# Kernel optimization log

Measured on AMD Instinct MI355X. Metric: run time of the kernel, lower is better.

## Reference

```python
import jax, jax.numpy as jnp
import numpy as np

B, D, K, M1, M2 = 256, 128, 32, 64, 32   # batch, n_nodes, K copies, dims[1], dims[2]
H1, H2, L = 128, 64, 32                   # pivae_dims


def setup_inputs() -> dict:
    key = jax.random.key(0)
    ks = iter(jax.random.split(key, 32))

    def rn(shape, scale):
        return jax.random.normal(next(ks), shape, dtype=jnp.float32) * scale

    x = jax.random.normal(next(ks), (B, D), dtype=jnp.float32)

    # per-node fc1 weights: [D, M1, D]; bounds force nonneg with zero diag column
    W1_pos = jnp.abs(rn((D, M1, D), 1.0 / np.sqrt(D)))
    W1_neg = jnp.abs(rn((D, M1, D), 1.0 / np.sqrt(D)))
    eye = jnp.eye(D, dtype=jnp.float32)[:, None, :]   # zero out W[j,:,j]
    W1_pos = W1_pos * (1.0 - eye)
    W1_neg = W1_neg * (1.0 - eye)
    b1_pos = rn((D, M1), 0.02)
    b1_neg = rn((D, M1), 0.02)

    # LocallyConnected stacks: weight [K, m_in, m_out]
    lc1_w = rn((K, M1, M2), 1.0 / np.sqrt(M1)); lc1_b = rn((K, M2), 0.02)
    lc2_w = rn((K, M2, 1), 1.0 / np.sqrt(M2));  lc2_b = rn((K, 1), 0.02)

    # per-sample beta Linear(k,1): weights [B, K], bias [B]
    beta_w = rn((B, K), 1.0 / np.sqrt(K)); beta_b = rn((B,), 0.02)

    # VAE params (encoder -> mu/logvar -> decoder), stored as (in,out) matrices
    enc1_w = rn((K, H1), 1.0 / np.sqrt(K));  enc1_b = jnp.zeros((H1,), jnp.float32)
    enc2_w = rn((H1, H2), 1.0 / np.sqrt(H1)); enc2_b = jnp.zeros((H2,), jnp.float32)
    mu_w = rn((H2, L), 1.0 / np.sqrt(H2));    mu_b = jnp.zeros((L,), jnp.float32)
    lv_w = rn((H2, L), 1.0 / np.sqrt(H2));    lv_b = jnp.zeros((L,), jnp.float32)
    dec1_w = rn((L, H2), 1.0 / np.sqrt(L));   dec1_b = jnp.zeros((H2,), jnp.float32)
    dec2_w = rn((H2, H1), 1.0 / np.sqrt(H2)); dec2_b = jnp.zeros((H1,), jnp.float32)
    dec3_w = rn((H1, K), 1.0 / np.sqrt(H1));  dec3_b = jnp.zeros((K,), jnp.float32)

    eps = jax.random.normal(next(ks), (B, L), dtype=jnp.float32)  # reparam noise

    return dict(x=x, W1_pos=W1_pos, W1_neg=W1_neg, b1_pos=b1_pos, b1_neg=b1_neg,
                lc1_w=lc1_w, lc1_b=lc1_b, lc2_w=lc2_w, lc2_b=lc2_b,
                beta_w=beta_w, beta_b=beta_b,
                enc1_w=enc1_w, enc1_b=enc1_b, enc2_w=enc2_w, enc2_b=enc2_b,
                mu_w=mu_w, mu_b=mu_b, lv_w=lv_w, lv_b=lv_b,
                dec1_w=dec1_w, dec1_b=dec1_b, dec2_w=dec2_w, dec2_b=dec2_b,
                dec3_w=dec3_w, dec3_b=dec3_b, eps=eps)


def reference(x, W1_pos, W1_neg, b1_pos, b1_neg, lc1_w, lc1_b, lc2_w, lc2_b,
              beta_w, beta_b, enc1_w, enc1_b, enc2_w, enc2_b, mu_w, mu_b,
              lv_w, lv_b, dec1_w, dec1_b, dec2_w, dec2_b, dec3_w, dec3_b, eps):
    b, d = x.shape
    k = lc1_w.shape[0]

    # fused per-node fc1: (pos - neg) applied to x with column j zeroed, all j at once
    W1 = W1_pos - W1_neg                      # [D, M1, D]
    b1 = b1_pos - b1_neg                      # [D, M1]
    full = jnp.einsum('bi,jhi->bjh', x, W1)   # as if no column were zeroed
    diagW = jnp.einsum('jhj->jh', W1)         # [D, M1] column-j weight of node j
    phi = full - x[:, :, None] * diagW[None] + b1[None]   # [B, D, M1]

    # expand to K copies, run sigmoid + LocallyConnected stack
    h = jnp.broadcast_to(phi[:, :, None, :], (b, d, k, phi.shape[-1]))
    h = jnp.einsum('bdkm,kmn->bdkn', jax.nn.sigmoid(h), lc1_w) + lc1_b   # [B,D,K,M2]
    h = jnp.einsum('bdkm,kmn->bdkn', jax.nn.sigmoid(h), lc2_w) + lc2_b   # [B,D,K,1]
    last_phi_x = h[..., 0]                    # [B, D, K]

    # per-sample beta projection (batched over B)
    y1 = jnp.einsum('bdk,bk->bd', last_phi_x, beta_w) + beta_b[:, None]

    # VAE on the stacked beta weights [B, K]
    e = jax.nn.relu(beta_w @ enc1_w + enc1_b)
    e = jax.nn.relu(e @ enc2_w + enc2_b)
    mu = e @ mu_w + mu_b
    logvar = e @ lv_w + lv_b
    z = mu + eps * jnp.exp(0.5 * logvar)
    dh = jax.nn.relu(z @ dec1_w + dec1_b)
    dh = jax.nn.relu(dh @ dec2_w + dec2_b)
    recon = dh @ dec3_w + dec3_b              # [B, K]

    y2 = jnp.einsum('bdk,bk->bd', last_phi_x, recon) + beta_b[:, None]
    return (y1, y2, mu, logvar)
```

## Files before the change

kernel.cpp:

```cpp
#include <hip/hip_runtime.h>
#include <stdint.h>

#define BB 256
#define DD 128
#define KK 32
#define MM1 64
#define MM2 32

typedef __attribute__((ext_vector_type(8))) short bf16x8;
typedef __attribute__((ext_vector_type(4))) float f32x4;

__device__ __forceinline__ short f2b(float f) {
  uint32_t u = __builtin_bit_cast(uint32_t, f);
  u += 0x7FFFu + ((u >> 16) & 1u);
  return (short)(u >> 16);
}
__device__ __forceinline__ float sigmoidf_fast(float xv) {
  return __builtin_amdgcn_rcpf(1.0f + __expf(-xv));
}

__global__ __launch_bounds__(128) void vae_kernel(
    const float* __restrict__ betaw,
    const float* __restrict__ enc1w, const float* __restrict__ enc1b,
    const float* __restrict__ enc2w, const float* __restrict__ enc2b,
    const float* __restrict__ muw,  const float* __restrict__ mub,
    const float* __restrict__ lvw,  const float* __restrict__ lvb,
    const float* __restrict__ dec1w, const float* __restrict__ dec1b,
    const float* __restrict__ dec2w, const float* __restrict__ dec2b,
    const float* __restrict__ dec3w, const float* __restrict__ dec3b,
    const float* __restrict__ eps,
    float* __restrict__ mu_out, float* __restrict__ lv_out,
    float* __restrict__ recon_out)
{
  const int b = blockIdx.x, t = threadIdx.x;
  __shared__ float bw[KK], e1[128], e2[64], zz[32], d1s[64];
  if (t < KK) bw[t] = betaw[b * KK + t];
  __syncthreads();
  {
    float acc = enc1b[t];
    #pragma unroll
    for (int k = 0; k < KK; ++k) acc = fmaf(bw[k], enc1w[k * 128 + t], acc);
    e1[t] = fmaxf(acc, 0.f);
  }
  __syncthreads();
  if (t < 64) {
    float a2 = enc2b[t];
    #pragma unroll 8
    for (int h = 0; h < 128; ++h) a2 = fmaf(e1[h], enc2w[h * 64 + t], a2);
    e2[t] = fmaxf(a2, 0.f);
  }
  __syncthreads();
  if (t < 32) {
    float m = mub[t], l = lvb[t];
    #pragma unroll 8
    for (int h = 0; h < 64; ++h) {
      float e = e2[h];
      m = fmaf(e, muw[h * 32 + t], m);
      l = fmaf(e, lvw[h * 32 + t], l);
    }
    mu_out[b * 32 + t] = m;
    lv_out[b * 32 + t] = l;
    zz[t] = fmaf(eps[b * 32 + t], __expf(0.5f * l), m);
  }
  __syncthreads();
  if (t < 64) {
    float a3 = dec1b[t];
    #pragma unroll
    for (int l = 0; l < 32; ++l) a3 = fmaf(zz[l], dec1w[l * 64 + t], a3);
    d1s[t] = fmaxf(a3, 0.f);
  }
  __syncthreads();
  float d2v;
  {
    float a4 = dec2b[t];
    #pragma unroll 8
    for (int h = 0; h < 64; ++h) a4 = fmaf(d1s[h], dec2w[h * 128 + t], a4);
    d2v = fmaxf(a4, 0.f);
  }
  __syncthreads();
  __shared__ float d2s[128];
  d2s[t] = d2v;
  __syncthreads();
  if (t < 32) {
    float a5 = dec3b[t];
    #pragma unroll 8
    for (int h = 0; h < 128; ++h) a5 = fmaf(d2s[h], dec3w[h * 32 + t], a5);
    recon_out[b * 32 + t] = a5;
  }
}

__global__ __launch_bounds__(512) void main_kernel(
    const float* __restrict__ x,
    const float* __restrict__ W1p, const float* __restrict__ W1n,
    const float* __restrict__ b1p, const float* __restrict__ b1n,
    const float* __restrict__ lc1w, const float* __restrict__ lc1b,
    const float* __restrict__ lc2w, const float* __restrict__ lc2b,
    const float* __restrict__ betaw, const float* __restrict__ betab,
    const float* __restrict__ recon,
    float* __restrict__ out)
{
  const int bx = blockIdx.x;
  const int d = bx >> 1;
  const int b0 = (bx & 1) * 128;
  const int tid = threadIdx.x;
  const int wave = tid >> 6;
  const int lane = tid & 63;

  __shared__ __align__(16) short sS[128 * 64];
  __shared__ __align__(16) float betaS[128 * 32];
  __shared__ __align__(16) float reconS[128 * 32];
  __shared__ __align__(16) float lc2S[KK * MM2];
  __shared__ __align__(16) float lc1bS[KK * MM2];
  __shared__ float lc2bS[KK];
  __shared__ float b1S[MM1];
  __shared__ __align__(16) short uni[32768];

  {
    const float4* xsrc = (const float4*)(x + b0 * DD);
    for (int e = tid; e < 4096; e += 512) {
      float4 v = xsrc[e];
      int row = e >> 5;
      int i = (e & 31) * 4;
      int ib = i & ~7, il = i & 7;
      short4 o; o.x = f2b(v.x); o.y = f2b(v.y); o.z = f2b(v.z); o.w = f2b(v.w);
      *(short4*)&uni[row * 128 + (ib ^ ((row & 7) << 3)) + il] = o;
    }
    const float4* wp = (const float4*)(W1p + d * MM1 * DD);
    const float4* wn = (const float4*)(W1n + d * MM1 * DD);
    for (int e = tid; e < 2048; e += 512) {
      float4 p = wp[e], n = wn[e];
      int m = e >> 5;
      int i = (e & 31) * 4;
      int ib = i & ~7, il = i & 7;
      short4 o; o.x = f2b(p.x - n.x); o.y = f2b(p.y - n.y);
      o.z = f2b(p.z - n.z); o.w = f2b(p.w - n.w);
      *(short4*)&uni[16384 + m * 128 + (ib ^ ((m & 7) << 3)) + il] = o;
    }
    if (tid < MM1) b1S[tid] = b1p[d * MM1 + tid] - b1n[d * MM1 + tid];
    const float4* bws = (const float4*)(betaw + b0 * KK);
    const float4* rcs = (const float4*)(recon + b0 * KK);
    for (int e = tid; e < 1024; e += 512) {
      ((float4*)betaS)[e]  = bws[e];
      ((float4*)reconS)[e] = rcs[e];
    }
    if (tid < 256) {
      ((float4*)lc2S)[tid]  = ((const float4*)lc2w)[tid];
      ((float4*)lc1bS)[tid] = ((const float4*)lc1b)[tid];
    }
    if (tid < KK) lc2bS[tid] = lc2b[tid];
  }
  __syncthreads();

  {
    const int row = wave * 16 + (lane & 15);
    const int kof = (lane >> 4) * 8;
    const int rsw = (row & 7) << 3;
    bf16x8 a[4];
    #pragma unroll
    for (int ks = 0; ks < 4; ++ks)
      a[ks] = *(const bf16x8*)&uni[row * 128 + ((ks * 32 + kof) ^ rsw)];
    #pragma unroll
    for (int ct = 0; ct < 4; ++ct) {
      const int m = ct * 16 + (lane & 15);
      const int msw = (m & 7) << 3;
      f32x4 acc = {0.f, 0.f, 0.f, 0.f};
      #pragma unroll
      for (int ks = 0; ks < 4; ++ks) {
        bf16x8 bf = *(const bf16x8*)&uni[16384 + m * 128 + ((ks * 32 + kof) ^ msw)];
        acc = __builtin_amdgcn_mfma_f32_16x16x32_bf16(a[ks], bf, acc, 0, 0, 0);
      }
      const float bias = b1S[m];
      #pragma unroll
      for (int r = 0; r < 4; ++r) {
        int bb = wave * 16 + (lane >> 4) * 4 + r;
        float s = sigmoidf_fast(acc[r] + bias);
        int mhi = m & ~7, mlo = m & 7;
        sS[bb * 64 + (mhi ^ ((bb & 7) << 3)) + mlo] = f2b(s);
      }
    }
  }
  __syncthreads();

  float y1a[4] = {0, 0, 0, 0}, y2a[4] = {0, 0, 0, 0};
  bf16x8 sa[2];
  {
    const int row = wave * 16 + (lane & 15);
    const int kofl = (lane >> 4) * 8;
    const int rsw = (row & 7) << 3;
    sa[0] = *(const bf16x8*)&sS[row * 64 + ((0 + kofl) ^ rsw)];
    sa[1] = *(const bf16x8*)&sS[row * 64 + ((32 + kofl) ^ rsw)];
  }
  const int n0 = lane & 15;
  const int kof = (lane >> 4) * 8;
  #pragma unroll 1
  for (int kh = 0; kh < 2; ++kh) {
    __syncthreads();
    {
      const float* src = lc1w + kh * 32768;
      for (int e = tid; e < 32768; e += 512) {
        int kq = e >> 11;
        int m = (e >> 5) & 63;
        int n = e & 31;
        int cp = kq * 32 + n;
        uni[cp * 64 + ((m & ~7) ^ ((cp & 7) << 3)) + (m & 7)] = f2b(src[e]);
      }
    }
    __syncthreads();
    for (int kk = 0; kk < 16; ++kk) {
      const int k = kh * 16 + kk;
      const int c0 = kk * 32 + n0, c1 = c0 + 16;
      const float bi0 = lc1bS[k * 32 + n0], bi1 = lc1bS[k * 32 + n0 + 16];
      f32x4 acc0 = {bi0, bi0, bi0, bi0}, acc1 = {bi1, bi1, bi1, bi1};
      #pragma unroll
      for (int mh = 0; mh < 2; ++mh) {
        int mb = mh * 32 + kof;
        bf16x8 bf0 = *(const bf16x8*)&uni[c0 * 64 + (mb ^ ((c0 & 7) << 3))];
        bf16x8 bf1 = *(const bf16x8*)&uni[c1 * 64 + (mb ^ ((c1 & 7) << 3))];
        acc0 = __builtin_amdgcn_mfma_f32_16x16x32_bf16(sa[mh], bf0, acc0, 0, 0, 0);
        acc1 = __builtin_amdgcn_mfma_f32_16x16x32_bf16(sa[mh], bf1, acc1, 0, 0, 0);
      }
      const float w0 = lc2S[k * 32 + n0], w1 = lc2S[k * 32 + n0 + 16];
      float v[4];
      #pragma unroll
      for (int r = 0; r < 4; ++r)
        v[r] = fmaf(sigmoidf_fast(acc0[r]), w0, sigmoidf_fast(acc1[r]) * w1);
      #pragma unroll
      for (int msk = 1; msk <= 8; msk <<= 1) {
        #pragma unroll
        for (int r = 0; r < 4; ++r) v[r] += __shfl_xor(v[r], msk, 64);
      }
      const float l2b = lc2bS[k];
      #pragma unroll
      for (int r = 0; r < 4; ++r) {
        int bb = wave * 16 + (lane >> 4) * 4 + r;
        float h2 = v[r] + l2b;
        y1a[r] = fmaf(h2, betaS[bb * 32 + k], y1a[r]);
        y2a[r] = fmaf(h2, reconS[bb * 32 + k], y2a[r]);
      }
    }
  }

  if ((lane & 15) == 0) {
    #pragma unroll
    for (int r = 0; r < 4; ++r) {
      int row = b0 + wave * 16 + (lane >> 4) * 4 + r;
      float bconst = betab[row];
      out[row * DD + d] = y1a[r] + bconst;
      out[BB * DD + row * DD + d] = y2a[r] + bconst;
    }
  }
}

extern "C" void kernel_launch(void* const* d_in, const int* in_sizes, int n_in,
                              void* d_out, int out_size, void* d_ws, size_t ws_size,
                              hipStream_t stream) {
  const float* x     = (const float*)d_in[0];
  const float* W1p   = (const float*)d_in[1];
  const float* W1n   = (const float*)d_in[2];
  const float* b1p   = (const float*)d_in[3];
  const float* b1n   = (const float*)d_in[4];
  const float* lc1w  = (const float*)d_in[5];
  const float* lc1b  = (const float*)d_in[6];
  const float* lc2w  = (const float*)d_in[7];
  const float* lc2b  = (const float*)d_in[8];
  const float* betaw = (const float*)d_in[9];
  const float* betab = (const float*)d_in[10];
  const float* enc1w = (const float*)d_in[11];
  const float* enc1b = (const float*)d_in[12];
  const float* enc2w = (const float*)d_in[13];
  const float* enc2b = (const float*)d_in[14];
  const float* muw   = (const float*)d_in[15];
  const float* mub   = (const float*)d_in[16];
  const float* lvw   = (const float*)d_in[17];
  const float* lvb   = (const float*)d_in[18];
  const float* dec1w = (const float*)d_in[19];
  const float* dec1b = (const float*)d_in[20];
  const float* dec2w = (const float*)d_in[21];
  const float* dec2b = (const float*)d_in[22];
  const float* dec3w = (const float*)d_in[23];
  const float* dec3b = (const float*)d_in[24];
  const float* eps   = (const float*)d_in[25];

  float* out   = (float*)d_out;
  float* recon = (float*)d_ws;

  float* mu_out = out + BB * DD * 2;
  float* lv_out = mu_out + BB * 32;

  vae_kernel<<<dim3(BB), dim3(128), 0, stream>>>(
      betaw, enc1w, enc1b, enc2w, enc2b, muw, mub, lvw, lvb,
      dec1w, dec1b, dec2w, dec2b, dec3w, dec3b, eps,
      mu_out, lv_out, recon);

  main_kernel<<<dim3(256), dim3(512), 0, stream>>>(
      x, W1p, W1n, b1p, b1n, lc1w, lc1b, lc2w, lc2b,
      betaw, betab, recon, out);
}
```

Before: 166.4 us.

## Add prep kernel for bf16 conversions and restructure main kernel over finer grid

Adds a prep kernel that converts W1, x and lc1 weights to bf16 once, pre-transposes beta/recon, and folds biases into log2e-scaled constants so the sigmoid becomes a single exp2 plus rcp. The main kernel now runs 1024 blocks of 256 threads, each covering 32 batch rows per node. It splits the K dimension across waves, streams lc1 fragments straight from global memory with register double-buffering, and finishes with a cross-wave reduction in shared memory. This removes the redundant per-block conversion of lc1w and W1 into LDS. The costs are an extra launch, a workspace round trip, and more global/L2 traffic for the lc1 fragments.

```diff
diff --git a/kernel.cpp b/kernel.cpp
--- a/kernel.cpp
+++ b/kernel.cpp
@@ -10,13 +10,56 @@
 typedef __attribute__((ext_vector_type(8))) short bf16x8;
 typedef __attribute__((ext_vector_type(4))) float f32x4;
 
+#define LOG2E 1.44269504088896f
+
+
 __device__ __forceinline__ short f2b(float f) {
   uint32_t u = __builtin_bit_cast(uint32_t, f);
   u += 0x7FFFu + ((u >> 16) & 1u);
   return (short)(u >> 16);
 }
-__device__ __forceinline__ float sigmoidf_fast(float xv) {
-  return __builtin_amdgcn_rcpf(1.0f + __expf(-xv));
+__device__ __forceinline__ float sigm_pre(float acc, float cpre) {
+  return __builtin_amdgcn_rcpf(
+      1.0f + __builtin_amdgcn_exp2f(fmaf(acc, -LOG2E, cpre)));
+}
+
+__global__ __launch_bounds__(256) void prep_kernel(
+    const float* __restrict__ x, const float* __restrict__ W1p,
+    const float* __restrict__ W1n, const float* __restrict__ b1p,
+    const float* __restrict__ b1n, const float* __restrict__ lc1w,
+    const float* __restrict__ lc1b, const float* __restrict__ lc2b,
+    const float* __restrict__ betaw, char* __restrict__ ws)
+{
+  const int tid = blockIdx.x * 256 + threadIdx.x;
+
+  {
+    float4 a = ((const float4*)W1p)[tid];
+    float4 b = ((const float4*)W1n)[tid];
+    short4 s;
+    s.x = f2b(a.x - b.x); s.y = f2b(a.y - b.y);
+    s.z = f2b(a.z - b.z); s.w = f2b(a.w - b.w);
+    ((short4*)(ws + 303104))[tid] = s;
+  }
+  if (tid < 8192) {
+    float4 v = ((const float4*)x)[tid];
+    short4 s;
+    s.x = f2b(v.x); s.y = f2b(v.y); s.z = f2b(v.z); s.w = f2b(v.w);
+    ((short4*)(ws + 65536))[tid] = s;
+  }
+  if (tid < 65536) {
+    int k = tid >> 11, n = (tid >> 6) & 31, m = tid & 63;
+    ((short*)(ws + 131072))[tid] = f2b(lc1w[k * 2048 + m * 32 + n]);
+  }
+  if (tid < 8192) {
+    ((float*)(ws + 32768))[tid] = betaw[(tid & 255) * 32 + (tid >> 8)];
+  }
+  if (tid < 1024) {
+    ((float*)(ws + 262144))[tid] = -lc1b[tid] * LOG2E;
+  }
+  if (tid < 32) { ((float*)(ws + 266240))[tid] = 0.25f * lc2b[tid]; }
+  if (tid < 8192) {
+    ((float*)(ws + 270336))[tid] = -(b1p[tid] - b1n[tid]) * LOG2E;
+  }
 }
 
 __global__ __launch_bounds__(128) void vae_kernel(
@@ -30,224 +73,208 @@
     const float* __restrict__ dec3w, const float* __restrict__ dec3b,
     const float* __restrict__ eps,
     float* __restrict__ mu_out, float* __restrict__ lv_out,
-    float* __restrict__ recon_out)
+    float* __restrict__ reconT)
 {
   const int b = blockIdx.x, t = threadIdx.x;
-  __shared__ float bw[KK], e1[128], e2[64], zz[32], d1s[64];
+  __shared__ float bw[KK], e1[128], e2[64], zz[32], d1s[64], d2s[128];
   if (t < KK) bw[t] = betaw[b * KK + t];
   __syncthreads();
   {
-    float acc = enc1b[t];
+    float a0 = enc1b[t], a1 = 0.f;
     #pragma unroll
-    for (int k = 0; k < KK; ++k) acc = fmaf(bw[k], enc1w[k * 128 + t], acc);
-    e1[t] = fmaxf(acc, 0.f);
+    for (int k = 0; k < KK; k += 2) {
+      a0 = fmaf(bw[k], enc1w[k * 128 + t], a0);
+      a1 = fmaf(bw[k + 1], enc1w[(k + 1) * 128 + t], a1);
+    }
+    e1[t] = fmaxf(a0 + a1, 0.f);
   }
   __syncthreads();
   if (t < 64) {
-    float a2 = enc2b[t];
+    float a0 = enc2b[t], a1 = 0.f, a2 = 0.f, a3 = 0.f;
     #pragma unroll 8
-    for (int h = 0; h < 128; ++h) a2 = fmaf(e1[h], enc2w[h * 64 + t], a2);
-    e2[t] = fmaxf(a2, 0.f);
+    for (int h = 0; h < 128; h += 4) {
+      a0 = fmaf(e1[h], enc2w[h * 64 + t], a0);
+      a1 = fmaf(e1[h + 1], enc2w[(h + 1) * 64 + t], a1);
+      a2 = fmaf(e1[h + 2], enc2w[(h + 2) * 64 + t], a2);
+      a3 = fmaf(e1[h + 3], enc2w[(h + 3) * 64 + t], a3);
+    }
+    e2[t] = fmaxf((a0 + a1) + (a2 + a3), 0.f);
   }
   __syncthreads();
   if (t < 32) {
-    float m = mub[t], l = lvb[t];
+    float m0 = mub[t], m1 = 0.f, l0 = lvb[t], l1 = 0.f;
     #pragma unroll 8
-    for (int h = 0; h < 64; ++h) {
-      float e = e2[h];
-      m = fmaf(e, muw[h * 32 + t], m);
-      l = fmaf(e, lvw[h * 32 + t], l);
-    }
+    for (int h = 0; h < 64; h += 2) {
+      float ea = e2[h], eb = e2[h + 1];
+      m0 = fmaf(ea, muw[h * 32 + t], m0);
+      m1 = fmaf(eb, muw[(h + 1) * 32 + t], m1);
+      l0 = fmaf(ea, lvw[h * 32 + t], l0);
+      l1 = fmaf(eb, lvw[(h + 1) * 32 + t], l1);
+    }
+    float m = m0 + m1, l = l0 + l1;
     mu_out[b * 32 + t] = m;
     lv_out[b * 32 + t] = l;
     zz[t] = fmaf(eps[b * 32 + t], __expf(0.5f * l), m);
   }
   __syncthreads();
   if (t < 64) {
-    float a3 = dec1b[t];
+    float a0 = dec1b[t], a1 = 0.f;
     #pragma unroll
-    for (int l = 0; l < 32; ++l) a3 = fmaf(zz[l], dec1w[l * 64 + t], a3);
-    d1s[t] = fmaxf(a3, 0.f);
-  }
-  __syncthreads();
-  float d2v;
+    for (int l = 0; l < 32; l += 2) {
+      a0 = fmaf(zz[l], dec1w[l * 64 + t], a0);
+      a1 = fmaf(zz[l + 1], dec1w[(l + 1) * 64 + t], a1);
+    }
+    d1s[t] = fmaxf(a0 + a1, 0.f);
+  }
+  __syncthreads();
   {
-    float a4 = dec2b[t];
+    float a0 = dec2b[t], a1 = 0.f, a2 = 0.f, a3 = 0.f;
     #pragma unroll 8
-    for (int h = 0; h < 64; ++h) a4 = fmaf(d1s[h], dec2w[h * 128 + t], a4);
-    d2v = fmaxf(a4, 0.f);
-  }
-  __syncthreads();
-  __shared__ float d2s[128];
-  d2s[t] = d2v;
+    for (int h = 0; h < 64; h += 4) {
+      a0 = fmaf(d1s[h], dec2w[h * 128 + t], a0);
+      a1 = fmaf(d1s[h + 1], dec2w[(h + 1) * 128 + t], a1);
+      a2 = fmaf(d1s[h + 2], dec2w[(h + 2) * 128 + t], a2);
+      a3 = fmaf(d1s[h + 3], dec2w[(h + 3) * 128 + t], a3);
+    }
+    d2s[t] = fmaxf((a0 + a1) + (a2 + a3), 0.f);
+  }
   __syncthreads();
   if (t < 32) {
-    float a5 = dec3b[t];
+    float a0 = dec3b[t], a1 = 0.f, a2 = 0.f, a3 = 0.f;
     #pragma unroll 8
-    for (int h = 0; h < 128; ++h) a5 = fmaf(d2s[h], dec3w[h * 32 + t], a5);
-    recon_out[b * 32 + t] = a5;
-  }
-}
-
-__global__ __launch_bounds__(512) void main_kernel(
-    const float* __restrict__ x,
-    const float* __restrict__ W1p, const float* __restrict__ W1n,
-    const float* __restrict__ b1p, const float* __restrict__ b1n,
-    const float* __restrict__ lc1w, const float* __restrict__ lc1b,
-    const float* __restrict__ lc2w, const float* __restrict__ lc2b,
-    const float* __restrict__ betaw, const float* __restrict__ betab,
-    const float* __restrict__ recon,
-    float* __restrict__ out)
+    for (int h = 0; h < 128; h += 4) {
+      a0 = fmaf(d2s[h], dec3w[h * 32 + t], a0);
+      a1 = fmaf(d2s[h + 1], dec3w[(h + 1) * 32 + t], a1);
+      a2 = fmaf(d2s[h + 2], dec3w[(h + 2) * 32 + t], a2);
+      a3 = fmaf(d2s[h + 3], dec3w[(h + 3) * 32 + t], a3);
+    }
+    reconT[t * BB + b] = (a0 + a1) + (a2 + a3);
+  }
+}
+
+__global__ __launch_bounds__(256) void main_kernel(
+    const float* __restrict__ lc2w, const float* __restrict__ betab,
+    const char* __restrict__ ws, float* __restrict__ out)
 {
   const int bx = blockIdx.x;
-  const int d = bx >> 1;
-  const int b0 = (bx & 1) * 128;
+  const int d = bx >> 3;
+  const int bg = bx & 7;
   const int tid = threadIdx.x;
-  const int wave = tid >> 6;
-  const int lane = tid & 63;
-
-  __shared__ __align__(16) short sS[128 * 64];
-  __shared__ __align__(16) float betaS[128 * 32];
-  __shared__ __align__(16) float reconS[128 * 32];
-  __shared__ __align__(16) float lc2S[KK * MM2];
-  __shared__ __align__(16) float lc1bS[KK * MM2];
-  __shared__ float lc2bS[KK];
-  __shared__ float b1S[MM1];
-  __shared__ __align__(16) short uni[32768];
+  const int wave = tid >> 6, lane = tid & 63;
+  const int g = lane >> 4, l15 = lane & 15;
+  const int gb0 = bg * 32 + l15, gb1 = gb0 + 16;
+
+  const short* __restrict__ xbf   = (const short*)(ws + 65536);
+  const short* __restrict__ lc1T  = (const short*)(ws + 131072);
+  const float* __restrict__ lc1bs = (const float*)(ws + 262144);
+  const float* __restrict__ lc2bq = (const float*)(ws + 266240);
+  const float* __restrict__ b1s   = (const float*)(ws + 270336) + d * MM1;
+  const short* __restrict__ w1bf  = (const short*)(ws + 303104) + d * (MM1 * DD);
+  const float* __restrict__ betaT = (const float*)(ws + 32768);
+  const float* __restrict__ recT  = (const float*)(ws + 0);
+
+  __shared__ short sS[32 * 64];
+  __shared__ float yred[4][64];
 
   {
-    const float4* xsrc = (const float4*)(x + b0 * DD);
-    for (int e = tid; e < 4096; e += 512) {
-      float4 v = xsrc[e];
-      int row = e >> 5;
-      int i = (e & 31) * 4;
-      int ib = i & ~7, il = i & 7;
-      short4 o; o.x = f2b(v.x); o.y = f2b(v.y); o.z = f2b(v.z); o.w = f2b(v.w);
-      *(short4*)&uni[row * 128 + (ib ^ ((row & 7) << 3)) + il] = o;
-    }
-    const float4* wp = (const float4*)(W1p + d * MM1 * DD);
-    const float4* wn = (const float4*)(W1n + d * MM1 * DD);
-    for (int e = tid; e < 2048; e += 512) {
-      float4 p = wp[e], n = wn[e];
-      int m = e >> 5;
-      int i = (e & 31) * 4;
-      int ib = i & ~7, il = i & 7;
-      short4 o; o.x = f2b(p.x - n.x); o.y = f2b(p.y - n.y);
-      o.z = f2b(p.z - n.z); o.w = f2b(p.w - n.w);
-      *(short4*)&uni[16384 + m * 128 + (ib ^ ((m & 7) << 3)) + il] = o;
-    }
-    if (tid < MM1) b1S[tid] = b1p[d * MM1 + tid] - b1n[d * MM1 + tid];
-    const float4* bws = (const float4*)(betaw + b0 * KK);
-    const float4* rcs = (const float4*)(recon + b0 * KK);
-    for (int e = tid; e < 1024; e += 512) {
-      ((float4*)betaS)[e]  = bws[e];
-      ((float4*)reconS)[e] = rcs[e];
-    }
-    if (tid < 256) {
-      ((float4*)lc2S)[tid]  = ((const float4*)lc2w)[tid];
-      ((float4*)lc1bS)[tid] = ((const float4*)lc1b)[tid];
-    }
-    if (tid < KK) lc2bS[tid] = lc2b[tid];
-  }
-  __syncthreads();
-
-  {
-    const int row = wave * 16 + (lane & 15);
-    const int kof = (lane >> 4) * 8;
-    const int rsw = (row & 7) << 3;
-    bf16x8 a[4];
+    bf16x8 wbv[4];
+    const int m = wave * 16 + l15;
     #pragma unroll
     for (int ks = 0; ks < 4; ++ks)
-      a[ks] = *(const bf16x8*)&uni[row * 128 + ((ks * 32 + kof) ^ rsw)];
+      wbv[ks] = *(const bf16x8*)(w1bf + m * DD + ks * 32 + g * 8);
+    const float cpre = b1s[m];
     #pragma unroll
-    for (int ct = 0; ct < 4; ++ct) {
-      const int m = ct * 16 + (lane & 15);
-      const int msw = (m & 7) << 3;
+    for (int rt = 0; rt < 2; ++rt) {
       f32x4 acc = {0.f, 0.f, 0.f, 0.f};
       #pragma unroll
       for (int ks = 0; ks < 4; ++ks) {
-        bf16x8 bf = *(const bf16x8*)&uni[16384 + m * 128 + ((ks * 32 + kof) ^ msw)];
-        acc = __builtin_amdgcn_mfma_f32_16x16x32_bf16(a[ks], bf, acc, 0, 0, 0);
+        bf16x8 xa = *(const bf16x8*)(xbf + (bg * 32 + rt * 16 + l15) * DD +
+                                     ks * 32 + g * 8);
+        acc = __builtin_amdgcn_mfma_f32_16x16x32_bf16(xa, wbv[ks], acc, 0, 0, 0);
       }
-      const float bias = b1S[m];
       #pragma unroll
       for (int r = 0; r < 4; ++r) {
-        int bb = wave * 16 + (lane >> 4) * 4 + r;
-        float s = sigmoidf_fast(acc[r] + bias);
-        int mhi = m & ~7, mlo = m & 7;
-        sS[bb * 64 + (mhi ^ ((bb & 7) << 3)) + mlo] = f2b(s);
+        const int bl = rt * 16 + g * 4 + r;
+        float s = sigm_pre(acc[r], cpre);
+        sS[bl * 64 + ((m & ~7) ^ ((bl & 7) << 3)) + (m & 7)] = f2b(s);
       }
     }
   }
   __syncthreads();
 
-  float y1a[4] = {0, 0, 0, 0}, y2a[4] = {0, 0, 0, 0};
-  bf16x8 sa[2];
-  {
-    const int row = wave * 16 + (lane & 15);
-    const int kofl = (lane >> 4) * 8;
-    const int rsw = (row & 7) << 3;
-    sa[0] = *(const bf16x8*)&sS[row * 64 + ((0 + kofl) ^ rsw)];
-    sa[1] = *(const bf16x8*)&sS[row * 64 + ((32 + kofl) ^ rsw)];
-  }
-  const int n0 = lane & 15;
-  const int kof = (lane >> 4) * 8;
-  #pragma unroll 1
-  for (int kh = 0; kh < 2; ++kh) {
-    __syncthreads();
-    {
-      const float* src = lc1w + kh * 32768;
-      for (int e = tid; e < 32768; e += 512) {
-        int kq = e >> 11;
-        int m = (e >> 5) & 63;
-        int n = e & 31;
-        int cp = kq * 32 + n;
-        uni[cp * 64 + ((m & ~7) ^ ((cp & 7) << 3)) + (m & 7)] = f2b(src[e]);
-      }
-    }
-    __syncthreads();
-    for (int kk = 0; kk < 16; ++kk) {
-      const int k = kh * 16 + kk;
-      const int c0 = kk * 32 + n0, c1 = c0 + 16;
-      const float bi0 = lc1bS[k * 32 + n0], bi1 = lc1bS[k * 32 + n0 + 16];
-      f32x4 acc0 = {bi0, bi0, bi0, bi0}, acc1 = {bi1, bi1, bi1, bi1};
-      #pragma unroll
-      for (int mh = 0; mh < 2; ++mh) {
-        int mb = mh * 32 + kof;
-        bf16x8 bf0 = *(const bf16x8*)&uni[c0 * 64 + (mb ^ ((c0 & 7) << 3))];
-        bf16x8 bf1 = *(const bf16x8*)&uni[c1 * 64 + (mb ^ ((c1 & 7) << 3))];
-        acc0 = __builtin_amdgcn_mfma_f32_16x16x32_bf16(sa[mh], bf0, acc0, 0, 0, 0);
-        acc1 = __builtin_amdgcn_mfma_f32_16x16x32_bf16(sa[mh], bf1, acc1, 0, 0, 0);
-      }
-      const float w0 = lc2S[k * 32 + n0], w1 = lc2S[k * 32 + n0 + 16];
-      float v[4];
-      #pragma unroll
-      for (int r = 0; r < 4; ++r)
-        v[r] = fmaf(sigmoidf_fast(acc0[r]), w0, sigmoidf_fast(acc1[r]) * w1);
-      #pragma unroll
-      for (int msk = 1; msk <= 8; msk <<= 1) {
-        #pragma unroll
-        for (int r = 0; r < 4; ++r) v[r] += __shfl_xor(v[r], msk, 64);
-      }
-      const float l2b = lc2bS[k];
-      #pragma unroll
-      for (int r = 0; r < 4; ++r) {
-        int bb = wave * 16 + (lane >> 4) * 4 + r;
-        float h2 = v[r] + l2b;
-        y1a[r] = fmaf(h2, betaS[bb * 32 + k], y1a[r]);
-        y2a[r] = fmaf(h2, reconS[bb * 32 + k], y2a[r]);
-      }
-    }
-  }
-
-  if ((lane & 15) == 0) {
-    #pragma unroll
-    for (int r = 0; r < 4; ++r) {
-      int row = b0 + wave * 16 + (lane >> 4) * 4 + r;
-      float bconst = betab[row];
-      out[row * DD + d] = y1a[r] + bconst;
-      out[BB * DD + row * DD + d] = y2a[r] + bconst;
-    }
+  const bf16x8 sa0 = *(const bf16x8*)&sS[l15 * 64 + ((g * 8) ^ ((l15 & 7) << 3))];
+  const bf16x8 sa1 = *(const bf16x8*)&sS[l15 * 64 + ((32 + g * 8) ^ ((l15 & 7) << 3))];
+  const bf16x8 sa2 = *(const bf16x8*)&sS[(16 + l15) * 64 + ((g * 8) ^ ((l15 & 7) << 3))];
+  const bf16x8 sa3 = *(const bf16x8*)&sS[(16 + l15) * 64 + ((32 + g * 8) ^ ((l15 & 7) << 3))];
+
+  float y1a = 0.f, y2a = 0.f, y1b = 0.f, y2b = 0.f;
+  bf16x8 A0a, A1a, A2a, A3a, A0b, A1b, A2b, A3b;
+
+#define PREFA(kk, S) { \
+    const short* ap = lc1T + (kk) * 2048 + l15 * 64 + g * 8; \
+    A0##S = *(const bf16x8*)(ap); \
+    A1##S = *(const bf16x8*)(ap + 32); \
+    A2##S = *(const bf16x8*)(ap + 1024); \
+    A3##S = *(const bf16x8*)(ap + 1056); }
+
+#define COMPUTE(kk, S) { \
+    f32x4 acc00 = {0,0,0,0}, acc01 = {0,0,0,0}; \
+    f32x4 acc10 = {0,0,0,0}, acc11 = {0,0,0,0}; \
+    acc00 = __builtin_amdgcn_mfma_f32_16x16x32_bf16(A0##S, sa0, acc00, 0, 0, 0); \
+    acc00 = __builtin_amdgcn_mfma_f32_16x16x32_bf16(A1##S, sa1, acc00, 0, 0, 0); \
+    acc01 = __builtin_amdgcn_mfma_f32_16x16x32_bf16(A0##S, sa2, acc01, 0, 0, 0); \
+    acc01 = __builtin_amdgcn_mfma_f32_16x16x32_bf16(A1##S, sa3, acc01, 0, 0, 0); \
+    acc10 = __builtin_amdgcn_mfma_f32_16x16x32_bf16(A2##S, sa0, acc10, 0, 0, 0); \
+    acc10 = __builtin_amdgcn_mfma_f32_16x16x32_bf16(A3##S, sa1, acc10, 0, 0, 0); \
+    acc11 = __builtin_amdgcn_mfma_f32_16x16x32_bf16(A2##S, sa2, acc11, 0, 0, 0); \
+    acc11 = __builtin_amdgcn_mfma_f32_16x16x32_bf16(A3##S, sa3, acc11, 0, 0, 0); \
+    f32x4 w0 = *(const f32x4*)(lc2w + (kk) * 32 + g * 4); \
+    f32x4 w1 = *(const f32x4*)(lc2w + (kk) * 32 + 16 + g * 4); \
+    f32x4 c0 = *(const f32x4*)(lc1bs + (kk) * 32 + g * 4); \
+    f32x4 c1 = *(const f32x4*)(lc1bs + (kk) * 32 + 16 + g * 4); \
+    float va = lc2bq[kk], vb = va; \
+    _Pragma("unroll") \
+    for (int r = 0; r < 4; ++r) { \
+      va = fmaf(sigm_pre(acc00[r], c0[r]), w0[r], va); \
+      va = fmaf(sigm_pre(acc10[r], c1[r]), w1[r], va); \
+      vb = fmaf(sigm_pre(acc01[r], c0[r]), w0[r], vb); \
+      vb = fmaf(sigm_pre(acc11[r], c1[r]), w1[r], vb); \
+    } \
+    y1a = fmaf(va, betaT[(kk) * BB + gb0], y1a); \
+    y2a = fmaf(va, recT[(kk) * BB + gb0], y2a); \
+    y1b = fmaf(vb, betaT[(kk) * BB + gb1], y1b); \
+    y2b = fmaf(vb, recT[(kk) * BB + gb1], y2b); }
+
+  const int k0 = wave * 8;
+  PREFA(k0, a);
+  #pragma unroll
+  for (int kk = 0; kk < 8; kk += 2) {
+    PREFA(k0 + kk + 1, b);
+    COMPUTE(k0 + kk, a);
+    if (kk < 6) PREFA(k0 + kk + 2, a);
+    COMPUTE(k0 + kk + 1, b);
+  }
+#undef PREFA
+#undef COMPUTE
+
+  y1a += __shfl_xor(y1a, 16, 64); y1a += __shfl_xor(y1a, 32, 64);
+  y2a += __shfl_xor(y2a, 16, 64); y2a += __shfl_xor(y2a, 32, 64);
+  y1b += __shfl_xor(y1b, 16, 64); y1b += __shfl_xor(y1b, 32, 64);
+  y2b += __shfl_xor(y2b, 16, 64); y2b += __shfl_xor(y2b, 32, 64);
+
+  if (g == 0) {
+    yred[wave][l15 * 2 + 0] = y1a;
+    yred[wave][l15 * 2 + 1] = y2a;
+    yred[wave][32 + l15 * 2 + 0] = y1b;
+    yred[wave][32 + l15 * 2 + 1] = y2b;
+  }
+  __syncthreads();
+  if (tid < 64) {
+    float s = yred[0][tid] + yred[1][tid] + yred[2][tid] + yred[3][tid];
+    const int rt = tid >> 5, q = tid & 31, l = q >> 1, o = q & 1;
+    const int b = bg * 32 + rt * 16 + l;
+    s += betab[b];
+    out[o * (BB * DD) + b * DD + d] = s;
   }
 }
 
@@ -281,18 +308,20 @@
   const float* dec3b = (const float*)d_in[24];
   const float* eps   = (const float*)d_in[25];
 
-  float* out   = (float*)d_out;
-  float* recon = (float*)d_ws;
-
+  float* out    = (float*)d_out;
+  char*  ws     = (char*)d_ws;
+  float* reconT = (float*)ws;
   float* mu_out = out + BB * DD * 2;
   float* lv_out = mu_out + BB * 32;
+
+  prep_kernel<<<dim3(1024), dim3(256), 0, stream>>>(
+      x, W1p, W1n, b1p, b1n, lc1w, lc1b, lc2b, betaw, ws);
 
   vae_kernel<<<dim3(BB), dim3(128), 0, stream>>>(
       betaw, enc1w, enc1b, enc2w, enc2b, muw, mub, lvw, lvb,
       dec1w, dec1b, dec2w, dec2b, dec3w, dec3b, eps,
-      mu_out, lv_out, recon);
-
-  main_kernel<<<dim3(256), dim3(512), 0, stream>>>(
-      x, W1p, W1n, b1p, b1n, lc1w, lc1b, lc2w, lc2b,
-      betaw, betab, recon, out);
-}
+      mu_out, lv_out, reconT);
+
+  main_kernel<<<dim3(1024), dim3(256), 0, stream>>>(
+      lc2w, betab, (const char*)ws, out);
+}
```

Result: faster. 148.9 us (-10.5%).
